# Performance work log

Measured on AMD Instinct MI355X. Metric: run time of the kernel, lower is better.

The kernel has to match this reference:

```python
import jax, jax.numpy as jnp
import numpy as np

BATCH, SEQ, D_IN, D_OUT = 32, 1024, 128, 128
NEG_SLOPE = 0.1


def setup_inputs() -> dict:
    key = jax.random.key(0)
    k1, k2, k3, k4 = jax.random.split(key, 4)
    nodes = jax.random.normal(k1, (BATCH, SEQ, D_IN), dtype=jnp.float32)
    adjacent = jax.random.randint(k2, (BATCH, SEQ, SEQ), 0, 2, dtype=jnp.int32)
    W = jax.random.normal(k3, (D_IN, D_OUT), dtype=jnp.float32) / np.sqrt(D_IN)
    B = jax.random.normal(k4, (D_IN, D_OUT), dtype=jnp.float32) / np.sqrt(D_IN)
    return {"nodes": nodes, "adjacent": adjacent, "W": W, "B": B}


def reference(nodes, adjacent, W, B):
    # mask[b, out, in] = 1 if edge (out -> in) present
    mask = (adjacent != 0).astype(nodes.dtype)
    # counts[b, in] = in-degree (number of 'out' neighbors pooled per target node)
    counts = mask.sum(axis=1)                               # [b, s_in]
    # segment-sum of neighbor features: pooled[b, in, d] = sum_out mask * nodes[b, out, d]
    pooled = jnp.einsum('boi,bod->bid', mask, nodes)        # [b, s_in, d]
    # mean over neighbors; nodes with zero degree get no pooled contribution
    pooled = jnp.where(counts[..., None] > 0,
                       pooled / jnp.maximum(counts, 1.0)[..., None],
                       jnp.zeros((), dtype=nodes.dtype))
    updated = nodes @ B + pooled @ W                        # [b, s, d_out]
    return jax.nn.leaky_relu(updated, negative_slope=NEG_SLOPE)
```

## Files before the change

### kernel.cpp

```cpp
#include <hip/hip_runtime.h>
#include <hip/hip_bf16.h>

#define SEQ 1024
#define DIM 128
#define NEG_SLOPE 0.1f

typedef __bf16 bf16x8 __attribute__((ext_vector_type(8)));
typedef float f32x4v __attribute__((ext_vector_type(4)));

__device__ __forceinline__ unsigned short bfb(float f) {
    __bf16 h = (__bf16)f;
    return __builtin_bit_cast(unsigned short, h);
}
__device__ __forceinline__ unsigned mpack(int x0, int x1) {
    unsigned m0 = (x0 != 0) ? 0x3F80u : 0u;
    unsigned m1 = (x1 != 0) ? 0x3F80u : 0u;
    return m0 | (m1 << 16);
}
__device__ __forceinline__ void bar() {
    asm volatile("s_waitcnt lgkmcnt(0)" ::: "memory");
    __builtin_amdgcn_s_barrier();
    __builtin_amdgcn_sched_barrier(0);
}

__global__ __launch_bounds__(256)
void wb_t(const float* __restrict__ W, const float* __restrict__ Bm,
          unsigned short* __restrict__ WT, unsigned short* __restrict__ BT) {
    const int gid = blockIdx.x * 256 + threadIdx.x;
    const int n = gid >> 7, k = gid & 127;
    WT[gid] = bfb(W[k * DIM + n]);
    BT[gid] = bfb(Bm[k * DIM + n]);
}

__global__ __launch_bounds__(256)
void nodes_t_kernel(const float* __restrict__ nodes, unsigned short* __restrict__ nodesT) {
    const int b  = blockIdx.x >> 4;
    const int o0 = (blockIdx.x & 15) << 6;
    __shared__ unsigned short T[DIM][66];

    const float* src = nodes + (size_t)b * SEQ * DIM;
    const int t = threadIdx.x & 31;
    const int g = threadIdx.x >> 5;

    float4 v[8];
    #pragma unroll
    for (int r = 0; r < 8; ++r)
        v[r] = *(const float4*)(src + (size_t)(o0 + g * 8 + r) * DIM + 4 * t);
    #pragma unroll
    for (int j = 0; j < 4; ++j) {
        #pragma unroll
        for (int p = 0; p < 4; ++p) {
            unsigned w = (unsigned)bfb(((const float*)&v[2 * p])[j]) |
                         ((unsigned)bfb(((const float*)&v[2 * p + 1])[j]) << 16);
            *(unsigned*)((unsigned char*)&T[0][0] + (size_t)(4 * t + j) * 132 + (g * 8 + 2 * p) * 2) = w;
        }
    }
    __syncthreads();
    const int d = threadIdx.x >> 1, h = threadIdx.x & 1;
    unsigned u[16];
    #pragma unroll
    for (int s = 0; s < 16; ++s)
        u[s] = *(const unsigned*)((const unsigned char*)&T[0][0] + (size_t)d * 132 + h * 64 + s * 4);
    unsigned short* dst = nodesT + (size_t)b * DIM * SEQ + (size_t)d * SEQ + o0 + h * 32;
    #pragma unroll
    for (int s = 0; s < 4; ++s) {
        uint4 q = make_uint4(u[4 * s], u[4 * s + 1], u[4 * s + 2], u[4 * s + 3]);
        *(uint4*)((unsigned char*)dst + s * 16) = q;
    }
}

__global__ __launch_bounds__(256)
void adj_pack(const int* __restrict__ adj, unsigned* __restrict__ packT) {
    const int b    = blockIdx.x >> 5;
    const int slab = blockIdx.x & 31;
    const int o0   = slab << 5;
    const int wave = threadIdx.x >> 6;
    const int lane = threadIdx.x & 63;
    __shared__ unsigned pk[32][33];

    const int* base = adj + (size_t)b * SEQ * SEQ;
    #pragma unroll
    for (int r = 0; r < 8; ++r) {
        const int* row = base + (size_t)(o0 + wave * 8 + r) * SEQ;
        int4 v[4];
        #pragma unroll
        for (int q = 0; q < 4; ++q)
            v[q] = *(const int4*)(row + q * 256 + lane * 4);
        #pragma unroll
        for (int q = 0; q < 4; ++q) {
            unsigned long long m0 = __ballot(v[q].x != 0);
            unsigned long long m1 = __ballot(v[q].y != 0);
            unsigned long long m2 = __ballot(v[q].z != 0);
            unsigned long long m3 = __ballot(v[q].w != 0);
            if (lane < 8) {
                const int sh = 8 * lane;
                unsigned w = ((unsigned)(m0 >> sh) & 0xFFu)
                           | (((unsigned)(m1 >> sh) & 0xFFu) << 8)
                           | (((unsigned)(m2 >> sh) & 0xFFu) << 16)
                           | (((unsigned)(m3 >> sh) & 0xFFu) << 24);
                pk[8 * q + lane][wave * 8 + r] = w;
            }
        }
    }
    __syncthreads();
    const int it = threadIdx.x >> 3, oos = (threadIdx.x & 7) * 4;
    uint4 w4 = make_uint4(pk[it][oos], pk[it][oos + 1], pk[it][oos + 2], pk[it][oos + 3]);
    *(uint4*)(packT + (size_t)b * 32 * SEQ + (size_t)it * SEQ + o0 + oos) = w4;
}

__device__ __forceinline__ bf16x8 expand8(const uint4 Wa, const uint4 Wb, int s) {
    union { unsigned u[4]; bf16x8 v; } r;
    r.u[0] = ((Wa.x >> s) & 1u) * 0x3F80u | ((((Wa.y >> s) & 1u) * 0x3F80u) << 16);
    r.u[1] = ((Wa.z >> s) & 1u) * 0x3F80u | ((((Wa.w >> s) & 1u) * 0x3F80u) << 16);
    r.u[2] = ((Wb.x >> s) & 1u) * 0x3F80u | ((((Wb.y >> s) & 1u) * 0x3F80u) << 16);
    r.u[3] = ((Wb.z >> s) & 1u) * 0x3F80u | ((((Wb.w >> s) & 1u) * 0x3F80u) << 16);
    return r.v;
}

__global__ __launch_bounds__(256, 4)
void gcn_fused(const float* __restrict__ nodes,
               const unsigned* __restrict__ packT,
               const unsigned short* __restrict__ nodesT,
               const unsigned short* __restrict__ WT,
               const unsigned short* __restrict__ BT,
               float* __restrict__ out)
{
    __shared__ union {
        unsigned pk[1024];
        unsigned short pooled[32][136];
    } u;

    const int bid   = blockIdx.x;
    const int xcd   = bid & 7;
    const int slot  = bid >> 3;
    const int batch = ((slot >> 5) << 3) | xcd;
    const int itile = slot & 31;
    const int i0    = itile << 5;

    const int tid  = threadIdx.x;
    const int wave = tid >> 6;
    const int lane = tid & 63;
    const int lrow = lane & 15;
    const int quad = lane >> 4;
    const int p0   = 8 * (lrow & 3) + (lrow >> 2);

    const float*          __restrict__ nodes_b = nodes  + (size_t)batch * SEQ * DIM;
    const unsigned*       __restrict__ pk_b    = packT  + (size_t)batch * 32 * SEQ + (size_t)itile * SEQ;
    const unsigned short* __restrict__ nT_b    = nodesT + (size_t)batch * DIM * SEQ;

    ((uint4*)u.pk)[tid] = ((const uint4*)pk_b)[tid];
    bar();

    f32x4v acc[2][2] = {};
    f32x4v acc_cnt[2] = {};
    bf16x8 ones;
    #pragma unroll
    for (int j = 0; j < 8; ++j) ones[j] = __builtin_bit_cast(__bf16, (unsigned short)0x3F80);

    bf16x8 bvA[4], bvB[4];

    auto load_bv = [&](int c, bf16x8 (&bv)[4]) {
        const unsigned short* pn = nT_b + (size_t)(wave * 32 + lrow) * SEQ + c * 64 + quad * 8;
        bv[0] = *(const bf16x8*)(pn);
        bv[1] = *(const bf16x8*)(pn + 16 * SEQ);
        bv[2] = *(const bf16x8*)(pn + 32);
        bv[3] = *(const bf16x8*)(pn + 16 * SEQ + 32);
    };
    auto compute = [&](int c, const bf16x8 (&bv)[4]) {
        #pragma unroll
        for (int kk = 0; kk < 2; ++kk) {
            const uint4 Wa = *(const uint4*)&u.pk[c * 64 + kk * 32 + quad * 8];
            const uint4 Wb = *(const uint4*)&u.pk[c * 64 + kk * 32 + quad * 8 + 4];
            bf16x8 av0 = expand8(Wa, Wb, p0);
            bf16x8 av1 = expand8(Wa, Wb, p0 + 4);
            acc[0][0] = __builtin_amdgcn_mfma_f32_16x16x32_bf16(av0, bv[2 * kk + 0], acc[0][0], 0, 0, 0);
            acc[0][1] = __builtin_amdgcn_mfma_f32_16x16x32_bf16(av0, bv[2 * kk + 1], acc[0][1], 0, 0, 0);
            acc[1][0] = __builtin_amdgcn_mfma_f32_16x16x32_bf16(av1, bv[2 * kk + 0], acc[1][0], 0, 0, 0);
            acc[1][1] = __builtin_amdgcn_mfma_f32_16x16x32_bf16(av1, bv[2 * kk + 1], acc[1][1], 0, 0, 0);
            acc_cnt[0] = __builtin_amdgcn_mfma_f32_16x16x32_bf16(av0, ones, acc_cnt[0], 0, 0, 0);
            acc_cnt[1] = __builtin_amdgcn_mfma_f32_16x16x32_bf16(av1, ones, acc_cnt[1], 0, 0, 0);
        }
    };

    load_bv(0, bvA);
    load_bv(1, bvB);
    for (int cc = 0; cc < 8; ++cc) {
        const int c0 = 2 * cc;
        compute(c0, bvA);
        if (c0 + 2 < 16) load_bv(c0 + 2, bvA);
        compute(c0 + 1, bvB);
        if (c0 + 3 < 16) load_bv(c0 + 3, bvB);
    }

    bar();

    #pragma unroll
    for (int mf = 0; mf < 2; ++mf) {
        #pragma unroll
        for (int r = 0; r < 4; ++r) {
            const int row = mf * 16 + quad * 4 + r;
            const float cnt = acc_cnt[mf][r];
            const float inv = (cnt > 0.5f) ? 1.0f / cnt : 0.0f;
            #pragma unroll
            for (int nf = 0; nf < 2; ++nf)
                u.pooled[row][wave * 32 + nf * 16 + lrow] = bfb(acc[mf][nf][r] * inv);
        }
    }
    bar();

    f32x4v acc2[2][2] = {};
    const int dn = wave * 32 + lrow;

    #pragma unroll
    for (int ks = 0; ks < 4; ++ks) {
        const int k0 = ks * 32 + quad * 8;
        bf16x8 av[2], bv2[2];
        #pragma unroll
        for (int mf = 0; mf < 2; ++mf)
            av[mf] = *(const bf16x8*)((const unsigned char*)&u.pooled[0][0] + (mf * 16 + lrow) * 272 + k0 * 2);
        #pragma unroll
        for (int nf = 0; nf < 2; ++nf)
            bv2[nf] = *(const bf16x8*)(WT + (size_t)(dn + nf * 16) * DIM + k0);
        #pragma unroll
        for (int mf = 0; mf < 2; ++mf)
            #pragma unroll
            for (int nf = 0; nf < 2; ++nf)
                acc2[mf][nf] = __builtin_amdgcn_mfma_f32_16x16x32_bf16(av[mf], bv2[nf], acc2[mf][nf], 0, 0, 0);
    }
    #pragma unroll
    for (int ks = 0; ks < 4; ++ks) {
        const int k0 = ks * 32 + quad * 8;
        bf16x8 av[2], bv2[2];
        #pragma unroll
        for (int mf = 0; mf < 2; ++mf) {
            const float* p = nodes_b + (size_t)(i0 + mf * 16 + lrow) * DIM + k0;
            const float4 f1 = *(const float4*)p;
            const float4 f2 = *(const float4*)(p + 4);
            av[mf][0] = (__bf16)f1.x; av[mf][1] = (__bf16)f1.y;
            av[mf][2] = (__bf16)f1.z; av[mf][3] = (__bf16)f1.w;
            av[mf][4] = (__bf16)f2.x; av[mf][5] = (__bf16)f2.y;
            av[mf][6] = (__bf16)f2.z; av[mf][7] = (__bf16)f2.w;
        }
        #pragma unroll
        for (int nf = 0; nf < 2; ++nf)
            bv2[nf] = *(const bf16x8*)(BT + (size_t)(dn + nf * 16) * DIM + k0);
        #pragma unroll
        for (int mf = 0; mf < 2; ++mf)
            #pragma unroll
            for (int nf = 0; nf < 2; ++nf)
                acc2[mf][nf] = __builtin_amdgcn_mfma_f32_16x16x32_bf16(av[mf], bv2[nf], acc2[mf][nf], 0, 0, 0);
    }

    float* out_b = out + (size_t)batch * SEQ * DIM;
    #pragma unroll
    for (int mf = 0; mf < 2; ++mf) {
        #pragma unroll
        for (int nf = 0; nf < 2; ++nf) {
            const int col = wave * 32 + nf * 16 + lrow;
            #pragma unroll
            for (int r = 0; r < 4; ++r) {
                const int row = i0 + mf * 16 + quad * 4 + r;
                const float x = acc2[mf][nf][r];
                out_b[(size_t)row * DIM + col] = (x > 0.0f) ? x : NEG_SLOPE * x;
            }
        }
    }
}

#define BUF_STRIDE 24576
#define NODES_OFF  8192
__device__ __forceinline__ int fb_swz(int row, int unit) {
    const int x  = row >> 2;
    const int fx = ((x & 3) | ((x & 1) << 2)) ^ ((x >> 2) & 7);
    return row * 128 + ((unit ^ fx) << 4);
}
__global__ __launch_bounds__(256, 2)
void gcn_fused_fb(const float* __restrict__ nodes, const int* __restrict__ adj,
                  const float* __restrict__ W, const float* __restrict__ Bm,
                  float* __restrict__ out)
{
    __shared__ alignas(16) unsigned char lds[2 * BUF_STRIDE];
    const int bid = blockIdx.x, xcd = bid & 7, slot = bid >> 3;
    const int batch = ((slot >> 4) << 3) | xcd, mtile = slot & 15, i0 = mtile << 6;
    const int tid = threadIdx.x, wave = tid >> 6, lane = tid & 63;
    const int wm = wave >> 1, wn = wave & 1, lrow = lane & 15, quad = lane >> 4;
    const int* __restrict__ adj_b = adj + (size_t)batch * SEQ * SEQ;
    const float* __restrict__ nodes_b = nodes + (size_t)batch * SEQ * DIM;
    const int a_row = (tid >> 4) * 4, a_col = (tid & 15) * 4;
    const int n_row = (tid >> 5) * 4, n_col = (tid & 31) * 4;
    const int m_unit = (tid >> 4) >> 1, m_sub = ((tid >> 4) & 1) * 8;
    const int n_unit = (tid >> 5) >> 1, n_sub = ((tid >> 5) & 1) * 8;
    f32x4v acc[2][4] = {}; f32x4v acc_cnt[2] = {};
    bf16x8 ones;
    #pragma unroll
    for (int j = 0; j < 8; ++j) ones[j] = __builtin_bit_cast(__bf16, (unsigned short)0x3F80);
    int4 A0[4], A1[4]; float4 N0[8], N1[8];
    auto load_chunk = [&](int o0, int4 (&A)[4], float4 (&N)[8]) {
        const int* pa = adj_b + (size_t)(o0 + a_row) * SEQ + (i0 + a_col);
        #pragma unroll
        for (int r = 0; r < 4; ++r) A[r] = *(const int4*)(pa + (size_t)r * SEQ);
        const float* pn = nodes_b + (size_t)(o0 + n_row) * DIM + n_col;
        #pragma unroll
        for (int it = 0; it < 2; ++it)
            #pragma unroll
            for (int r = 0; r < 4; ++r)
                N[it * 4 + r] = *(const float4*)(pn + (size_t)(it * 32 + r) * DIM);
    };
    auto write_lds = [&](int base, const int4 (&A)[4], const float4 (&N)[8]) {
        unsigned char* mb = lds + base; unsigned char* nb = lds + base + NODES_OFF;
        #pragma unroll
        for (int j = 0; j < 4; ++j) {
            uint2 w;
            w.x = mpack(((const int*)&A[0])[j], ((const int*)&A[1])[j]);
            w.y = mpack(((const int*)&A[2])[j], ((const int*)&A[3])[j]);
            *(uint2*)(mb + fb_swz(a_col + j, m_unit) + m_sub) = w;
        }
        #pragma unroll
        for (int it = 0; it < 2; ++it) {
            #pragma unroll
            for (int j = 0; j < 4; ++j) {
                uint2 w;
                w.x = (unsigned)bfb(((const float*)&N[it*4+0])[j]) | ((unsigned)bfb(((const float*)&N[it*4+1])[j]) << 16);
                w.y = (unsigned)bfb(((const float*)&N[it*4+2])[j]) | ((unsigned)bfb(((const float*)&N[it*4+3])[j]) << 16);
                *(uint2*)(nb + fb_swz(n_col + j, 4 * it + n_unit) + n_sub) = w;
            }
        }
    };
    auto compute = [&](int base) {
        const unsigned char* mb = lds + base; const unsigned char* nb = lds + base + NODES_OFF;
        #pragma unroll
        for (int kk = 0; kk < 2; ++kk) {
            bf16x8 av[2], bv[4];
            av[0] = *(const bf16x8*)(mb + fb_swz(wm * 32 + lrow, 4 * kk + quad));
            av[1] = *(const bf16x8*)(mb + fb_swz(wm * 32 + 16 + lrow, 4 * kk + quad));
            #pragma unroll
            for (int nf = 0; nf < 4; ++nf)
                bv[nf] = *(const bf16x8*)(nb + fb_swz(wn * 64 + nf * 16 + lrow, 4 * kk + quad));
            #pragma unroll
            for (int mf = 0; mf < 2; ++mf) {
                #pragma unroll
                for (int nf = 0; nf < 4; ++nf)
                    acc[mf][nf] = __builtin_amdgcn_mfma_f32_16x16x32_bf16(av[mf], bv[nf], acc[mf][nf], 0, 0, 0);
                acc_cnt[mf] = __builtin_amdgcn_mfma_f32_16x16x32_bf16(av[mf], ones, acc_cnt[mf], 0, 0, 0);
            }
        }
    };
    load_chunk(0, A0, N0); load_chunk(64, A1, N1);
    write_lds(0, A0, N0); load_chunk(128, A0, N0); bar();
    for (int cc = 0; cc < 8; ++cc) {
        const int c0 = cc * 2;
        compute(0); write_lds(BUF_STRIDE, A1, N1);
        if (c0 + 3 < 16) load_chunk((c0 + 3) * 64, A1, N1);
        bar();
        compute(BUF_STRIDE);
        if (c0 + 2 < 16) write_lds(0, A0, N0);
        if (c0 + 4 < 16) load_chunk((c0 + 4) * 64, A0, N0);
        bar();
    }
    unsigned short (*pooled)[136] = (unsigned short (*)[136])(void*)lds;
    #pragma unroll
    for (int mf = 0; mf < 2; ++mf)
        #pragma unroll
        for (int r = 0; r < 4; ++r) {
            const int row = wm * 32 + mf * 16 + quad * 4 + r;
            const float cnt = acc_cnt[mf][r];
            const float inv = (cnt > 0.5f) ? 1.0f / cnt : 0.0f;
            #pragma unroll
            for (int nf = 0; nf < 4; ++nf)
                pooled[row][wn * 64 + nf * 16 + lrow] = bfb(acc[mf][nf][r] * inv);
        }
    __syncthreads();
    f32x4v acc2[2][4] = {};
    const int d_b0 = wn * 64 + lrow;
    #pragma unroll
    for (int ks = 0; ks < 4; ++ks) {
        const int k0 = ks * 32 + quad * 8;
        bf16x8 av[2];
        #pragma unroll
        for (int mf = 0; mf < 2; ++mf)
            av[mf] = *(const bf16x8*)&pooled[wm * 32 + mf * 16 + lrow][k0];
        bf16x8 bv[4];
        const float* pw = W + (size_t)k0 * DIM + d_b0;
        #pragma unroll
        for (int nf = 0; nf < 4; ++nf)
            #pragma unroll
            for (int j = 0; j < 8; ++j) bv[nf][j] = (__bf16)pw[j * DIM + nf * 16];
        #pragma unroll
        for (int mf = 0; mf < 2; ++mf)
            #pragma unroll
            for (int nf = 0; nf < 4; ++nf)
                acc2[mf][nf] = __builtin_amdgcn_mfma_f32_16x16x32_bf16(av[mf], bv[nf], acc2[mf][nf], 0, 0, 0);
    }
    #pragma unroll
    for (int ks = 0; ks < 4; ++ks) {
        const int k0 = ks * 32 + quad * 8;
        bf16x8 av[2];
        #pragma unroll
        for (int mf = 0; mf < 2; ++mf) {
            const float* p = nodes_b + (size_t)(i0 + wm * 32 + mf * 16 + lrow) * DIM + k0;
            const float4 f1 = *(const float4*)p; const float4 f2 = *(const float4*)(p + 4);
            av[mf][0] = (__bf16)f1.x; av[mf][1] = (__bf16)f1.y;
            av[mf][2] = (__bf16)f1.z; av[mf][3] = (__bf16)f1.w;
            av[mf][4] = (__bf16)f2.x; av[mf][5] = (__bf16)f2.y;
            av[mf][6] = (__bf16)f2.z; av[mf][7] = (__bf16)f2.w;
        }
        bf16x8 bv[4];
        const float* pB = Bm + (size_t)k0 * DIM + d_b0;
        #pragma unroll
        for (int nf = 0; nf < 4; ++nf)
            #pragma unroll
            for (int j = 0; j < 8; ++j) bv[nf][j] = (__bf16)pB[j * DIM + nf * 16];
        #pragma unroll
        for (int mf = 0; mf < 2; ++mf)
            #pragma unroll
            for (int nf = 0; nf < 4; ++nf)
                acc2[mf][nf] = __builtin_amdgcn_mfma_f32_16x16x32_bf16(av[mf], bv[nf], acc2[mf][nf], 0, 0, 0);
    }
    float* out_b = out + (size_t)batch * SEQ * DIM;
    #pragma unroll
    for (int mf = 0; mf < 2; ++mf)
        #pragma unroll
        for (int nf = 0; nf < 4; ++nf) {
            const int col = wn * 64 + nf * 16 + lrow;
            #pragma unroll
            for (int r = 0; r < 4; ++r) {
                const int row = i0 + wm * 32 + mf * 16 + quad * 4 + r;
                const float x = acc2[mf][nf][r];
                out_b[(size_t)row * DIM + col] = (x > 0.0f) ? x : NEG_SLOPE * x;
            }
        }
}

extern "C" void kernel_launch(void* const* d_in, const int* in_sizes, int n_in,
                              void* d_out, int out_size, void* d_ws, size_t ws_size,
                              hipStream_t stream) {
    const float* nodes = (const float*)d_in[0];
    const int*   adj   = (const int*)d_in[1];
    const float* W     = (const float*)d_in[2];
    const float* Bm    = (const float*)d_in[3];
    float*       out   = (float*)d_out;

    const size_t PK_BYTES = (size_t)32 * 32 * SEQ * 4;
    const size_t NT_BYTES = (size_t)32 * DIM * SEQ * 2;
    const size_t WB_BYTES = (size_t)DIM * DIM * 2;
    const size_t NEED = PK_BYTES + NT_BYTES + 2 * WB_BYTES;

    if (d_ws != nullptr && ws_size >= NEED) {
        unsigned*       packT  = (unsigned*)d_ws;
        unsigned short* nodesT = (unsigned short*)((char*)d_ws + PK_BYTES);
        unsigned short* WT = (unsigned short*)((char*)d_ws + PK_BYTES + NT_BYTES);
        unsigned short* BT = (unsigned short*)((char*)d_ws + PK_BYTES + NT_BYTES + WB_BYTES);
        adj_pack<<<dim3(1024), dim3(256), 0, stream>>>(adj, packT);
        wb_t<<<dim3(64), dim3(256), 0, stream>>>(W, Bm, WT, BT);
        nodes_t_kernel<<<dim3(512), dim3(256), 0, stream>>>(nodes, nodesT);
        gcn_fused<<<dim3(1024), dim3(256), 0, stream>>>(nodes, packT, nodesT, WT, BT, out);
    } else {
        gcn_fused_fb<<<dim3(512), dim3(256), 0, stream>>>(nodes, adj, W, Bm, out);
    }
}
```

Measured before the change: 263.1 us.

## Fuse preprocessing and GCN kernels into one cooperative launch with grid sync

Merges the adjacency packing, nodes transpose, and W/B transpose kernels with the main fused GCN kernel into a single cooperative kernel that uses a grid-wide sync between the preprocessing and compute phases, with a fallback to separate launches if the cooperative launch fails. The aim is to remove kernel launch gaps and tail effects between the four launches. It also simplifies the mask expansion by shifting once and extracting two bits with masks instead of two variable shifts. The cost is that 1024 blocks at 256 threads must all be co-resident, and every block waits at the grid barrier.

```diff
diff --git a/kernel.cpp b/kernel.cpp
--- a/kernel.cpp
+++ b/kernel.cpp
@@ -1,5 +1,8 @@
 #include <hip/hip_runtime.h>
 #include <hip/hip_bf16.h>
+#include <hip/hip_cooperative_groups.h>
+
+namespace cg = cooperative_groups;
 
 #define SEQ 1024
 #define DIM 128
@@ -7,6 +10,13 @@
 
 typedef __bf16 bf16x8 __attribute__((ext_vector_type(8)));
 typedef float f32x4v __attribute__((ext_vector_type(4)));
+
+union LdsAll {
+    unsigned       pk_pack[32][33];
+    unsigned short T[DIM][66];
+    unsigned       pk_g[1024];
+    unsigned short pooled[32][136];
+};
 
 __device__ __forceinline__ unsigned short bfb(float f) {
     __bf16 h = (__bf16)f;
@@ -23,60 +33,14 @@
     __builtin_amdgcn_sched_barrier(0);
 }
 
-__global__ __launch_bounds__(256)
-void wb_t(const float* __restrict__ W, const float* __restrict__ Bm,
-          unsigned short* __restrict__ WT, unsigned short* __restrict__ BT) {
-    const int gid = blockIdx.x * 256 + threadIdx.x;
-    const int n = gid >> 7, k = gid & 127;
-    WT[gid] = bfb(W[k * DIM + n]);
-    BT[gid] = bfb(Bm[k * DIM + n]);
-}
-
-__global__ __launch_bounds__(256)
-void nodes_t_kernel(const float* __restrict__ nodes, unsigned short* __restrict__ nodesT) {
-    const int b  = blockIdx.x >> 4;
-    const int o0 = (blockIdx.x & 15) << 6;
-    __shared__ unsigned short T[DIM][66];
-
-    const float* src = nodes + (size_t)b * SEQ * DIM;
-    const int t = threadIdx.x & 31;
-    const int g = threadIdx.x >> 5;
-
-    float4 v[8];
-    #pragma unroll
-    for (int r = 0; r < 8; ++r)
-        v[r] = *(const float4*)(src + (size_t)(o0 + g * 8 + r) * DIM + 4 * t);
-    #pragma unroll
-    for (int j = 0; j < 4; ++j) {
-        #pragma unroll
-        for (int p = 0; p < 4; ++p) {
-            unsigned w = (unsigned)bfb(((const float*)&v[2 * p])[j]) |
-                         ((unsigned)bfb(((const float*)&v[2 * p + 1])[j]) << 16);
-            *(unsigned*)((unsigned char*)&T[0][0] + (size_t)(4 * t + j) * 132 + (g * 8 + 2 * p) * 2) = w;
-        }
-    }
-    __syncthreads();
-    const int d = threadIdx.x >> 1, h = threadIdx.x & 1;
-    unsigned u[16];
-    #pragma unroll
-    for (int s = 0; s < 16; ++s)
-        u[s] = *(const unsigned*)((const unsigned char*)&T[0][0] + (size_t)d * 132 + h * 64 + s * 4);
-    unsigned short* dst = nodesT + (size_t)b * DIM * SEQ + (size_t)d * SEQ + o0 + h * 32;
-    #pragma unroll
-    for (int s = 0; s < 4; ++s) {
-        uint4 q = make_uint4(u[4 * s], u[4 * s + 1], u[4 * s + 2], u[4 * s + 3]);
-        *(uint4*)((unsigned char*)dst + s * 16) = q;
-    }
-}
-
-__global__ __launch_bounds__(256)
-void adj_pack(const int* __restrict__ adj, unsigned* __restrict__ packT) {
-    const int b    = blockIdx.x >> 5;
-    const int slab = blockIdx.x & 31;
+__device__ __forceinline__ void do_adj_pack(const int* __restrict__ adj,
+                                            unsigned* __restrict__ packT,
+                                            int bid, int tid, LdsAll& L) {
+    const int b    = bid >> 5;
+    const int slab = bid & 31;
     const int o0   = slab << 5;
-    const int wave = threadIdx.x >> 6;
-    const int lane = threadIdx.x & 63;
-    __shared__ unsigned pk[32][33];
+    const int wave = tid >> 6;
+    const int lane = tid & 63;
 
     const int* base = adj + (size_t)b * SEQ * SEQ;
     #pragma unroll
@@ -98,46 +62,92 @@
                            | (((unsigned)(m1 >> sh) & 0xFFu) << 8)
                            | (((unsigned)(m2 >> sh) & 0xFFu) << 16)
                            | (((unsigned)(m3 >> sh) & 0xFFu) << 24);
-                pk[8 * q + lane][wave * 8 + r] = w;
+                L.pk_pack[8 * q + lane][wave * 8 + r] = w;
             }
         }
     }
     __syncthreads();
-    const int it = threadIdx.x >> 3, oos = (threadIdx.x & 7) * 4;
-    uint4 w4 = make_uint4(pk[it][oos], pk[it][oos + 1], pk[it][oos + 2], pk[it][oos + 3]);
+    const int it = tid >> 3, oos = (tid & 7) * 4;
+    uint4 w4 = make_uint4(L.pk_pack[it][oos], L.pk_pack[it][oos + 1],
+                          L.pk_pack[it][oos + 2], L.pk_pack[it][oos + 3]);
     *(uint4*)(packT + (size_t)b * 32 * SEQ + (size_t)it * SEQ + o0 + oos) = w4;
 }
 
-__device__ __forceinline__ bf16x8 expand8(const uint4 Wa, const uint4 Wb, int s) {
+__device__ __forceinline__ void do_nodes_t(const float* __restrict__ nodes,
+                                           unsigned short* __restrict__ nodesT,
+                                           int bid, int tid, LdsAll& L) {
+    const int b  = bid >> 4;
+    const int o0 = (bid & 15) << 6;
+    const float* src = nodes + (size_t)b * SEQ * DIM;
+    const int t = tid & 31;
+    const int g = tid >> 5;
+
+    float4 v[8];
+    #pragma unroll
+    for (int r = 0; r < 8; ++r)
+        v[r] = *(const float4*)(src + (size_t)(o0 + g * 8 + r) * DIM + 4 * t);
+    #pragma unroll
+    for (int j = 0; j < 4; ++j) {
+        #pragma unroll
+        for (int p = 0; p < 4; ++p) {
+            unsigned w = (unsigned)bfb(((const float*)&v[2 * p])[j]) |
+                         ((unsigned)bfb(((const float*)&v[2 * p + 1])[j]) << 16);
+            *(unsigned*)((unsigned char*)&L.T[0][0] + (size_t)(4 * t + j) * 132 + (g * 8 + 2 * p) * 2) = w;
+        }
+    }
+    __syncthreads();
+    const int d = tid >> 1, h = tid & 1;
+    unsigned u[16];
+    #pragma unroll
+    for (int s = 0; s < 16; ++s)
+        u[s] = *(const unsigned*)((const unsigned char*)&L.T[0][0] + (size_t)d * 132 + h * 64 + s * 4);
+    unsigned short* dst = nodesT + (size_t)b * DIM * SEQ + (size_t)d * SEQ + o0 + h * 32;
+    #pragma unroll
+    for (int s = 0; s < 4; ++s) {
+        uint4 q = make_uint4(u[4 * s], u[4 * s + 1], u[4 * s + 2], u[4 * s + 3]);
+        *(uint4*)((unsigned char*)dst + s * 16) = q;
+    }
+}
+
+__device__ __forceinline__ void do_wb(const float* __restrict__ W, const float* __restrict__ Bm,
+                                      unsigned short* __restrict__ WT, unsigned short* __restrict__ BT,
+                                      int wb_bid, int tid) {
+    const int gid = wb_bid * 256 + tid;
+    const int n = gid >> 7, k = gid & 127;
+    WT[gid] = bfb(W[k * DIM + n]);
+    BT[gid] = bfb(Bm[k * DIM + n]);
+}
+
+__device__ __forceinline__ bf16x8 expand_lo(const uint4 Sa, const uint4 Sb) {
     union { unsigned u[4]; bf16x8 v; } r;
-    r.u[0] = ((Wa.x >> s) & 1u) * 0x3F80u | ((((Wa.y >> s) & 1u) * 0x3F80u) << 16);
-    r.u[1] = ((Wa.z >> s) & 1u) * 0x3F80u | ((((Wa.w >> s) & 1u) * 0x3F80u) << 16);
-    r.u[2] = ((Wb.x >> s) & 1u) * 0x3F80u | ((((Wb.y >> s) & 1u) * 0x3F80u) << 16);
-    r.u[3] = ((Wb.z >> s) & 1u) * 0x3F80u | ((((Wb.w >> s) & 1u) * 0x3F80u) << 16);
+    r.u[0] = (Sa.x & 1u) * 0x3F80u | (Sa.y & 1u) * 0x3F800000u;
+    r.u[1] = (Sa.z & 1u) * 0x3F80u | (Sa.w & 1u) * 0x3F800000u;
+    r.u[2] = (Sb.x & 1u) * 0x3F80u | (Sb.y & 1u) * 0x3F800000u;
+    r.u[3] = (Sb.z & 1u) * 0x3F80u | (Sb.w & 1u) * 0x3F800000u;
     return r.v;
 }
-
-__global__ __launch_bounds__(256, 4)
-void gcn_fused(const float* __restrict__ nodes,
-               const unsigned* __restrict__ packT,
-               const unsigned short* __restrict__ nodesT,
-               const unsigned short* __restrict__ WT,
-               const unsigned short* __restrict__ BT,
-               float* __restrict__ out)
-{
-    __shared__ union {
-        unsigned pk[1024];
-        unsigned short pooled[32][136];
-    } u;
-
-    const int bid   = blockIdx.x;
+__device__ __forceinline__ bf16x8 expand_hi(const uint4 Sa, const uint4 Sb) {
+    union { unsigned u[4]; bf16x8 v; } r;
+    r.u[0] = (Sa.x & 16u) * 0x3F8u | (Sa.y & 16u) * 0x3F80000u;
+    r.u[1] = (Sa.z & 16u) * 0x3F8u | (Sa.w & 16u) * 0x3F80000u;
+    r.u[2] = (Sb.x & 16u) * 0x3F8u | (Sb.y & 16u) * 0x3F80000u;
+    r.u[3] = (Sb.z & 16u) * 0x3F8u | (Sb.w & 16u) * 0x3F80000u;
+    return r.v;
+}
+
+__device__ __forceinline__ void do_gcn(const float* __restrict__ nodes,
+                                       const unsigned* __restrict__ packT,
+                                       const unsigned short* __restrict__ nodesT,
+                                       const unsigned short* __restrict__ WT,
+                                       const unsigned short* __restrict__ BT,
+                                       float* __restrict__ out,
+                                       int bid, int tid, LdsAll& L) {
     const int xcd   = bid & 7;
     const int slot  = bid >> 3;
     const int batch = ((slot >> 5) << 3) | xcd;
     const int itile = slot & 31;
     const int i0    = itile << 5;
 
-    const int tid  = threadIdx.x;
     const int wave = tid >> 6;
     const int lane = tid & 63;
     const int lrow = lane & 15;
@@ -148,7 +158,7 @@
     const unsigned*       __restrict__ pk_b    = packT  + (size_t)batch * 32 * SEQ + (size_t)itile * SEQ;
     const unsigned short* __restrict__ nT_b    = nodesT + (size_t)batch * DIM * SEQ;
 
-    ((uint4*)u.pk)[tid] = ((const uint4*)pk_b)[tid];
+    ((uint4*)L.pk_g)[tid] = ((const uint4*)pk_b)[tid];
     bar();
 
     f32x4v acc[2][2] = {};
@@ -169,10 +179,13 @@
     auto compute = [&](int c, const bf16x8 (&bv)[4]) {
         #pragma unroll
         for (int kk = 0; kk < 2; ++kk) {
-            const uint4 Wa = *(const uint4*)&u.pk[c * 64 + kk * 32 + quad * 8];
-            const uint4 Wb = *(const uint4*)&u.pk[c * 64 + kk * 32 + quad * 8 + 4];
-            bf16x8 av0 = expand8(Wa, Wb, p0);
-            bf16x8 av1 = expand8(Wa, Wb, p0 + 4);
+            const uint4 Wa = *(const uint4*)&L.pk_g[c * 64 + kk * 32 + quad * 8];
+            const uint4 Wb = *(const uint4*)&L.pk_g[c * 64 + kk * 32 + quad * 8 + 4];
+            uint4 Sa, Sb;
+            Sa.x = Wa.x >> p0; Sa.y = Wa.y >> p0; Sa.z = Wa.z >> p0; Sa.w = Wa.w >> p0;
+            Sb.x = Wb.x >> p0; Sb.y = Wb.y >> p0; Sb.z = Wb.z >> p0; Sb.w = Wb.w >> p0;
+            bf16x8 av0 = expand_lo(Sa, Sb);
+            bf16x8 av1 = expand_hi(Sa, Sb);
             acc[0][0] = __builtin_amdgcn_mfma_f32_16x16x32_bf16(av0, bv[2 * kk + 0], acc[0][0], 0, 0, 0);
             acc[0][1] = __builtin_amdgcn_mfma_f32_16x16x32_bf16(av0, bv[2 * kk + 1], acc[0][1], 0, 0, 0);
             acc[1][0] = __builtin_amdgcn_mfma_f32_16x16x32_bf16(av1, bv[2 * kk + 0], acc[1][0], 0, 0, 0);
@@ -203,7 +216,7 @@
             const float inv = (cnt > 0.5f) ? 1.0f / cnt : 0.0f;
             #pragma unroll
             for (int nf = 0; nf < 2; ++nf)
-                u.pooled[row][wave * 32 + nf * 16 + lrow] = bfb(acc[mf][nf][r] * inv);
+                L.pooled[row][wave * 32 + nf * 16 + lrow] = bfb(acc[mf][nf][r] * inv);
         }
     }
     bar();
@@ -217,7 +230,7 @@
         bf16x8 av[2], bv2[2];
         #pragma unroll
         for (int mf = 0; mf < 2; ++mf)
-            av[mf] = *(const bf16x8*)((const unsigned char*)&u.pooled[0][0] + (mf * 16 + lrow) * 272 + k0 * 2);
+            av[mf] = *(const bf16x8*)((const unsigned char*)&L.pooled[0][0] + (mf * 16 + lrow) * 272 + k0 * 2);
         #pragma unroll
         for (int nf = 0; nf < 2; ++nf)
             bv2[nf] = *(const bf16x8*)(WT + (size_t)(dn + nf * 16) * DIM + k0);
@@ -265,6 +278,50 @@
             }
         }
     }
+}
+
+__global__ __launch_bounds__(256, 4)
+void gcn_all(const float* __restrict__ nodes, const int* __restrict__ adj,
+             const float* __restrict__ W, const float* __restrict__ Bm,
+             unsigned* __restrict__ packT, unsigned short* __restrict__ nodesT,
+             unsigned short* __restrict__ WT, unsigned short* __restrict__ BT,
+             float* __restrict__ out)
+{
+    __shared__ LdsAll L;
+    const int bid = blockIdx.x, tid = threadIdx.x;
+
+    do_adj_pack(adj, packT, bid, tid, L);
+    __syncthreads();
+    if (bid < 512)       do_nodes_t(nodes, nodesT, bid, tid, L);
+    else if (bid >= 960) do_wb(W, Bm, WT, BT, bid - 960, tid);
+
+    __threadfence();
+    cg::this_grid().sync();
+
+    do_gcn(nodes, packT, nodesT, WT, BT, out, bid, tid, L);
+}
+
+__global__ __launch_bounds__(256)
+void adj_pack_k(const int* __restrict__ adj, unsigned* __restrict__ packT) {
+    __shared__ LdsAll L;
+    do_adj_pack(adj, packT, blockIdx.x, threadIdx.x, L);
+}
+__global__ __launch_bounds__(256)
+void nodes_t_k(const float* __restrict__ nodes, unsigned short* __restrict__ nodesT) {
+    __shared__ LdsAll L;
+    do_nodes_t(nodes, nodesT, blockIdx.x, threadIdx.x, L);
+}
+__global__ __launch_bounds__(256)
+void wb_k(const float* __restrict__ W, const float* __restrict__ Bm,
+          unsigned short* __restrict__ WT, unsigned short* __restrict__ BT) {
+    do_wb(W, Bm, WT, BT, blockIdx.x, threadIdx.x);
+}
+__global__ __launch_bounds__(256, 4)
+void gcn_k(const float* __restrict__ nodes, const unsigned* __restrict__ packT,
+           const unsigned short* __restrict__ nodesT, const unsigned short* __restrict__ WT,
+           const unsigned short* __restrict__ BT, float* __restrict__ out) {
+    __shared__ LdsAll L;
+    do_gcn(nodes, packT, nodesT, WT, BT, out, blockIdx.x, threadIdx.x, L);
 }
 
 #define BUF_STRIDE 24576
@@ -450,10 +507,23 @@
         unsigned short* nodesT = (unsigned short*)((char*)d_ws + PK_BYTES);
         unsigned short* WT = (unsigned short*)((char*)d_ws + PK_BYTES + NT_BYTES);
         unsigned short* BT = (unsigned short*)((char*)d_ws + PK_BYTES + NT_BYTES + WB_BYTES);
-        adj_pack<<<dim3(1024), dim3(256), 0, stream>>>(adj, packT);
-        wb_t<<<dim3(64), dim3(256), 0, stream>>>(W, Bm, WT, BT);
-        nodes_t_kernel<<<dim3(512), dim3(256), 0, stream>>>(nodes, nodesT);
-        gcn_fused<<<dim3(1024), dim3(256), 0, stream>>>(nodes, packT, nodesT, WT, BT, out);
+
+        void* args[9];
+        args[0] = (void*)&nodes;  args[1] = (void*)&adj;
+        args[2] = (void*)&W;      args[3] = (void*)&Bm;
+        args[4] = (void*)&packT;  args[5] = (void*)&nodesT;
+        args[6] = (void*)&WT;     args[7] = (void*)&BT;
+        args[8] = (void*)&out;
+        hipError_t e = hipLaunchCooperativeKernel((const void*)gcn_all,
+                                                  dim3(1024), dim3(256),
+                                                  args, 0, stream);
+        if (e != hipSuccess) {
+            (void)hipGetLastError();
+            adj_pack_k<<<dim3(1024), dim3(256), 0, stream>>>(adj, packT);
+            wb_k<<<dim3(64), dim3(256), 0, stream>>>(W, Bm, WT, BT);
+            nodes_t_k<<<dim3(512), dim3(256), 0, stream>>>(nodes, nodesT);
+            gcn_k<<<dim3(1024), dim3(256), 0, stream>>>(nodes, packT, nodesT, WT, BT, out);
+        }
     } else {
         gcn_fused_fb<<<dim3(512), dim3(256), 0, stream>>>(nodes, adj, W, Bm, out);
     }
```

Result: slower. 523.7 us (+99.0%).
